# Performance work log

Hardware: AMD Instinct MI355X
Metric: run time of the kernel (lower is better)

## Reference

```python
import jax, jax.numpy as jnp
import numpy as np

B, S, D, H = 2, 2048, 1024, 16
HD = D // H  # head_size = 64

def setup_inputs() -> dict:
    key = jax.random.key(0)
    ks = jax.random.split(key, 8)
    sc = 0.02
    return {
        "q": jax.random.normal(ks[0], (B, S, D), jnp.float32),
        "k": jax.random.normal(ks[1], (B, S, D), jnp.float32),
        "v": jax.random.normal(ks[2], (B, S, D), jnp.float32),
        "padding_mask": jnp.zeros((B, 1, 1, S), jnp.float32),
        "Wq": jax.random.normal(ks[3], (D, D), jnp.float32) * sc,
        "bq": jnp.zeros((D,), jnp.float32),
        "Wk": jax.random.normal(ks[4], (D, D), jnp.float32) * sc,
        "bk": jnp.zeros((D,), jnp.float32),
        "Wv": jax.random.normal(ks[5], (D, D), jnp.float32) * sc,
        "bv": jnp.zeros((D,), jnp.float32),
        "Wo": jax.random.normal(ks[6], (D, D), jnp.float32) * sc,
        "bo": jnp.zeros((D,), jnp.float32),
    }

def reference(q, k, v, padding_mask, Wq, bq, Wk, bk, Wv, bv, Wo, bo):
    b = q.shape[0]
    qh = (q @ Wq + bq).reshape(b, -1, H, HD)
    kh = (k @ Wk + bk).reshape(b, -1, H, HD)
    vh = (v @ Wv + bv).reshape(b, -1, H, HD)
    # [B, H, Sq, Sk] scores, materialized as in the original
    qk = jnp.einsum('bjhd,bkhd->bhjk', qh, kh) / jnp.sqrt(jnp.float32(HD))
    qk = qk + padding_mask * -1e12
    attn = jax.nn.softmax(qk, axis=-1)
    qkv = jnp.einsum('bhjk,bkhd->bjhd', attn, vh).reshape(b, -1, D)
    return qkv @ Wo + bo
```

## Files before the change

kernel.cpp:

```cpp
#include <hip/hip_runtime.h>
#include <math.h>

typedef __bf16 bf16_t;
typedef __bf16 bf16x8 __attribute__((ext_vector_type(8)));
typedef __bf16 bf16x4v __attribute__((ext_vector_type(4)));
typedef float f32x4 __attribute__((ext_vector_type(4)));
typedef float f32x16 __attribute__((ext_vector_type(16)));

#define LOG2E 1.4426950408889634f
#define MBIAS_C (-1e12f * LOG2E)

#if __has_builtin(__builtin_amdgcn_exp2f)
#define EXP2F(x) __builtin_amdgcn_exp2f(x)
#else
#define EXP2F(x) exp2f(x)
#endif

typedef __attribute__((address_space(1))) const unsigned int g_u32;
typedef __attribute__((address_space(3))) unsigned int l_u32;
__device__ __forceinline__ void load_lds_16B(const void* g, void* l){
  __builtin_amdgcn_global_load_lds((g_u32*)g, (l_u32*)l, 16, 0, 0);
}

__device__ __forceinline__ f32x16 zero16(){
  f32x16 z;
  #pragma unroll
  for (int i = 0; i < 16; i++) z[i] = 0.f;
  return z;
}

typedef union { bf16x4v b4; uint2 u2; } pk8;
typedef union { uint2 h[2]; bf16x8 b8; } pk16;
typedef union { float4 f4[4]; f32x16 v; } cinit_t;

__global__ __launch_bounds__(256) void cast3_kernel(const float* __restrict__ q,
                                                    const float* __restrict__ k,
                                                    const float* __restrict__ v,
                                                    bf16_t* __restrict__ out){
  int z = blockIdx.y;
  const float* x = (z == 0) ? q : (z == 1) ? k : v;
  int i = blockIdx.x * 256 + threadIdx.x;
  float4 f = reinterpret_cast<const float4*>(x)[i];
  bf16x4v w;
  w[0] = (bf16_t)f.x; w[1] = (bf16_t)f.y; w[2] = (bf16_t)f.z; w[3] = (bf16_t)f.w;
  reinterpret_cast<bf16x4v*>(out + (size_t)z * 4194304)[i] = w;
}

__global__ __launch_bounds__(256) void mask_scale_kernel(const float* __restrict__ mask,
                                                         float* __restrict__ ms){
  int i = blockIdx.x * 256 + threadIdx.x;
  ms[i] = mask[i] * MBIAS_C;
}

__global__ __launch_bounds__(256) void wtrans4_kernel(const float* __restrict__ Wq,
                                                      const float* __restrict__ Wk,
                                                      const float* __restrict__ Wv,
                                                      const float* __restrict__ Wo,
                                                      bf16_t* __restrict__ Wcat,
                                                      bf16_t* __restrict__ Wot){
  __shared__ float T[32][33];
  int z = blockIdx.z;
  const float* W = (z == 0) ? Wq : (z == 1) ? Wk : (z == 2) ? Wv : Wo;
  bf16_t* dst = (z < 3) ? (Wcat + (size_t)z * 1024 * 1024) : Wot;
  int x = threadIdx.x, y = threadIdx.y;
  int k0 = blockIdx.y * 32, n0 = blockIdx.x * 32;
  #pragma unroll
  for (int i = 0; i < 4; i++) T[y + 8*i][x] = W[(size_t)(k0 + y + 8*i) * 1024 + n0 + x];
  __syncthreads();
  #pragma unroll
  for (int i = 0; i < 4; i++) dst[(size_t)(n0 + y + 8*i) * 1024 + k0 + x] = (bf16_t)T[x][y + 8*i];
}

__device__ __forceinline__ void qkv_epilogue(f32x4 (&acc)[4][4], int seg, int n0g, int m0,
                                             int wm, int wn, int l16, int lq,
                                             const float* bias, bf16_t* qp, bf16_t* kp,
                                             bf16_t* vh){
  bf16_t* Cp = (seg == 0) ? qp : (seg == 1) ? kp : vh;
  float scale = (seg == 0) ? 0.125f * LOG2E : 1.0f;
  #pragma unroll
  for (int ti = 0; ti < 4; ti++){
    #pragma unroll
    for (int tj = 0; tj < 4; tj++){
      int col = (n0g + wn + tj*16 + l16) & 1023;
      float bvv = bias[col];
      #pragma unroll
      for (int r = 0; r < 4; r++){
        int row = m0 + wm + ti*16 + lq*4 + r;
        Cp[(size_t)row * 1024 + col] = (bf16_t)((acc[ti][tj][r] + bvv) * scale);
      }
    }
  }
}

__global__ __launch_bounds__(256) void gemm_qkv_bf(const bf16_t* __restrict__ qkvin,
                                                   const bf16_t* __restrict__ Wcat,
                                                   const float* __restrict__ bq,
                                                   const float* __restrict__ bk,
                                                   const float* __restrict__ bv,
                                                   bf16_t* __restrict__ qp,
                                                   bf16_t* __restrict__ kp,
                                                   bf16_t* __restrict__ vh){
  const int K = 1024;
  __shared__ __align__(16) bf16_t As[128*32];
  __shared__ __align__(16) bf16_t Bs[128*32];
  int tid = threadIdx.x, wave = tid >> 6, lane = tid & 63;
  int l16 = lane & 15, lq = lane >> 4;
  int n0g = blockIdx.x * 128;
  int seg = n0g >> 10;
  const bf16_t* A   = qkvin + (size_t)seg * 4194304;
  const float* bias = (seg == 0) ? bq : (seg == 1) ? bk : bv;
  int m0 = blockIdx.y * 128;
  int wm = (wave >> 1) * 64, wn = (wave & 1) * 64;
  int cposR = lq ^ ((l16 >> 2) & 3);
  f32x4 acc[4][4] = {};
  for (int kt = 0; kt < K; kt += 32){
    __syncthreads();
    #pragma unroll
    for (int i = 0; i < 2; i++){
      int u = tid + 256*i;
      int r = u >> 2, cpos = u & 3, cg = cpos ^ ((r >> 2) & 3);
      int ldsoff = (wave*64 + 256*i) * 16;
      load_lds_16B(&A[(size_t)(m0 + r) * K + kt + cg*8], (char*)As + ldsoff);
      load_lds_16B(&Wcat[(size_t)(n0g + r) * K + kt + cg*8], (char*)Bs + ldsoff);
    }
    __syncthreads();
    bf16x8 af[4], bfr[4];
    #pragma unroll
    for (int t = 0; t < 4; t++) af[t]  = *reinterpret_cast<bf16x8*>(&As[(wm + t*16 + l16)*32 + cposR*8]);
    #pragma unroll
    for (int t = 0; t < 4; t++) bfr[t] = *reinterpret_cast<bf16x8*>(&Bs[(wn + t*16 + l16)*32 + cposR*8]);
    #pragma unroll
    for (int ti = 0; ti < 4; ti++)
      #pragma unroll
      for (int tj = 0; tj < 4; tj++)
        acc[ti][tj] = __builtin_amdgcn_mfma_f32_16x16x32_bf16(af[ti], bfr[tj], acc[ti][tj], 0, 0, 0);
  }
  qkv_epilogue(acc, seg, n0g, m0, wm, wn, l16, lq, bias, qp, kp, vh);
}

__global__ __launch_bounds__(256) void gemm_qkv_f32(const float* __restrict__ qi,
                                                    const float* __restrict__ ki,
                                                    const float* __restrict__ vi,
                                                    const bf16_t* __restrict__ Wcat,
                                                    const float* __restrict__ bq,
                                                    const float* __restrict__ bk,
                                                    const float* __restrict__ bv,
                                                    bf16_t* __restrict__ qp,
                                                    bf16_t* __restrict__ kp,
                                                    bf16_t* __restrict__ vh){
  const int K = 1024;
  __shared__ __align__(16) float  Asf[128*32];
  __shared__ __align__(16) bf16_t Bs[128*32];
  int tid = threadIdx.x, wave = tid >> 6, lane = tid & 63;
  int l16 = lane & 15, lq = lane >> 4;
  int n0g = blockIdx.x * 128;
  int seg = n0g >> 10;
  const float* A    = (seg == 0) ? qi : (seg == 1) ? ki : vi;
  const float* bias = (seg == 0) ? bq : (seg == 1) ? bk : bv;
  int m0 = blockIdx.y * 128;
  int wm = (wave >> 1) * 64, wn = (wave & 1) * 64;
  int cposR = lq ^ ((l16 >> 2) & 3);
  int ca0 = (2*lq)     ^ (l16 & 7);
  int ca1 = (2*lq + 1) ^ (l16 & 7);
  f32x4 acc[4][4] = {};
  for (int kt = 0; kt < K; kt += 32){
    __syncthreads();
    #pragma unroll
    for (int i = 0; i < 4; i++){
      int u = tid + 256*i;
      int r = u >> 3, cpos = u & 7, cg = cpos ^ (r & 7);
      load_lds_16B(&A[(size_t)(m0 + r) * K + kt + cg*4], (char*)Asf + (wave*64 + 256*i)*16);
    }
    #pragma unroll
    for (int i = 0; i < 2; i++){
      int u = tid + 256*i;
      int r = u >> 2, cpos = u & 3, cg = cpos ^ ((r >> 2) & 3);
      load_lds_16B(&Wcat[(size_t)(n0g + r) * K + kt + cg*8], (char*)Bs + (wave*64 + 256*i)*16);
    }
    __syncthreads();
    bf16x8 af[4], bfr[4];
    #pragma unroll
    for (int t = 0; t < 4; t++){
      int row = wm + t*16 + l16;
      f32x4 x0 = *reinterpret_cast<f32x4*>(&Asf[row*32 + ca0*4]);
      f32x4 x1 = *reinterpret_cast<f32x4*>(&Asf[row*32 + ca1*4]);
      bf16x8 a;
      a[0] = (bf16_t)x0[0]; a[1] = (bf16_t)x0[1]; a[2] = (bf16_t)x0[2]; a[3] = (bf16_t)x0[3];
      a[4] = (bf16_t)x1[0]; a[5] = (bf16_t)x1[1]; a[6] = (bf16_t)x1[2]; a[7] = (bf16_t)x1[3];
      af[t] = a;
    }
    #pragma unroll
    for (int t = 0; t < 4; t++) bfr[t] = *reinterpret_cast<bf16x8*>(&Bs[(wn + t*16 + l16)*32 + cposR*8]);
    #pragma unroll
    for (int ti = 0; ti < 4; ti++)
      #pragma unroll
      for (int tj = 0; tj < 4; tj++)
        acc[ti][tj] = __builtin_amdgcn_mfma_f32_16x16x32_bf16(af[ti], bfr[tj], acc[ti][tj], 0, 0, 0);
  }
  qkv_epilogue(acc, seg, n0g, m0, wm, wn, l16, lq, bias, qp, kp, vh);
}

__global__ __launch_bounds__(256) void gemm_out(const bf16_t* __restrict__ A,
                                                const bf16_t* __restrict__ Bt,
                                                const float* __restrict__ bias,
                                                float* __restrict__ C){
  const int K = 1024, N = 1024;
  __shared__ __align__(16) bf16_t As[128*64];
  __shared__ __align__(16) bf16_t Bs[64*64];
  int tid = threadIdx.x, wave = tid >> 6, lane = tid & 63;
  int l16 = lane & 15, lq = lane >> 4;
  int m0 = blockIdx.y * 128, n0 = blockIdx.x * 64;
  int wm = wave * 32;
  f32x4 acc[2][4] = {};
  for (int kt = 0; kt < K; kt += 64){
    __syncthreads();
    #pragma unroll
    for (int i = 0; i < 4; i++){
      int u = tid + 256*i;
      int r = u >> 3, cpos = u & 7, cg = cpos ^ (r & 7);
      load_lds_16B(&A[(size_t)(m0 + r) * K + kt + cg*8], (char*)As + (wave*64 + 256*i)*16);
    }
    #pragma unroll
    for (int i = 0; i < 2; i++){
      int u = tid + 256*i;
      int r = u >> 3, cpos = u & 7, cg = cpos ^ (r & 7);
      load_lds_16B(&Bt[(size_t)(n0 + r) * K + kt + cg*8], (char*)Bs + (wave*64 + 256*i)*16);
    }
    __syncthreads();
    #pragma unroll
    for (int kk = 0; kk < 2; kk++){
      bf16x8 af[2], bfr[4];
      #pragma unroll
      for (int t = 0; t < 2; t++){
        int row = wm + t*16 + l16, cpos = (kk*4 + lq) ^ (l16 & 7);
        af[t] = *reinterpret_cast<bf16x8*>(&As[row*64 + cpos*8]);
      }
      #pragma unroll
      for (int t = 0; t < 4; t++){
        int row = t*16 + l16, cpos = (kk*4 + lq) ^ (l16 & 7);
        bfr[t] = *reinterpret_cast<bf16x8*>(&Bs[row*64 + cpos*8]);
      }
      #pragma unroll
      for (int ti = 0; ti < 2; ti++)
        #pragma unroll
        for (int tj = 0; tj < 4; tj++)
          acc[ti][tj] = __builtin_amdgcn_mfma_f32_16x16x32_bf16(af[ti], bfr[tj], acc[ti][tj], 0, 0, 0);
    }
  }
  #pragma unroll
  for (int ti = 0; ti < 2; ti++){
    #pragma unroll
    for (int tj = 0; tj < 4; tj++){
      int col = n0 + tj*16 + l16;
      float bvv = bias[col];
      #pragma unroll
      for (int r = 0; r < 4; r++){
        int row = m0 + wm + ti*16 + lq*4 + r;
        C[(size_t)row * N + col] = acc[ti][tj][r] + bvv;
      }
    }
  }
}

__global__ __launch_bounds__(256) void vtrans_kernel(const bf16_t* __restrict__ vh,
                                                     bf16_t* __restrict__ Vt){
  __shared__ bf16_t T[64][72];
  int tid = threadIdx.x;
  int s0 = blockIdx.x * 64, h = blockIdx.y, b = blockIdx.z;
  #pragma unroll
  for (int i = 0; i < 2; i++){
    int u = tid + 256*i;
    int r = u >> 3, c = (u & 7) * 8;
    *reinterpret_cast<uint4*>(&T[r][c]) =
      *reinterpret_cast<const uint4*>(&vh[(size_t)(b*2048 + s0 + r) * 1024 + h*64 + c]);
  }
  __syncthreads();
  #pragma unroll
  for (int i = 0; i < 2; i++){
    int u = tid + 256*i;
    int d = u >> 3, cs = (u & 7) * 8;
    bf16_t t8[8];
    #pragma unroll
    for (int j = 0; j < 8; j++) t8[j] = T[cs + j][d];
    *reinterpret_cast<uint4*>(&Vt[(size_t)((b*16 + h)*64 + d) * 2048 + s0 + cs]) =
      *reinterpret_cast<uint4*>(t8);
  }
}

__global__ __launch_bounds__(256, 4) void attn_kernel(const bf16_t* __restrict__ qp,
                                                      const bf16_t* __restrict__ kp,
                                                      const bf16_t* __restrict__ vt,
                                                      const float* __restrict__ ms,
                                                      bf16_t* __restrict__ ctx){
  const int S = 2048, D = 1024, HD = 64;
  __shared__ __align__(16) char smem[33024];
  float* Lsum  = (float*)(smem + 32768);
  float* Opart = (float*)smem;
  int tid = threadIdx.x, wave = tid >> 6, lane = tid & 63;
  int l32 = lane & 31, H = lane >> 5;
  int qhalf = wave & 1, khalf = wave >> 1;
  int qt = blockIdx.x, h = blockIdx.y, b = blockIdx.z;
  const bf16_t* Qg = qp + (size_t)b*S*D + h*HD;
  const bf16_t* Kg = kp + (size_t)b*S*D + h*HD;
  const bf16_t* Vg = vt + (size_t)(b*16 + h)*HD*S;
  const float*  Mg = ms + (size_t)b*S;

  auto stage = [&](int kt, int bsel){
    char* Kd = smem + bsel*8192;
    char* Vd = smem + 16384 + bsel*8192;
    #pragma unroll
    for (int i = 0; i < 2; i++){
      int u = tid + 256*i;
      int r = u >> 3, c = u & 7, cg = c ^ (r & 7);
      int ldsoff = (wave*64 + 256*i) * 16;
      load_lds_16B(&Kg[(size_t)(kt + r) * D + cg*8], Kd + ldsoff);
      load_lds_16B(&Vg[(size_t)r * S + kt + cg*8], Vd + ldsoff);
    }
  };

  int qrow = qt*64 + qhalf*32 + l32;
  bf16x8 qf[4];
  #pragma unroll
  for (int s = 0; s < 4; s++)
    qf[s] = *reinterpret_cast<const bf16x8*>(&Qg[(size_t)qrow * D + s*16 + 8*H]);

  f32x16 o0 = zero16(), o1 = zero16(), lmm = zero16();
  int krow = khalf*32 + l32;

  pk16 ones;
  ones.h[0].x = 0x3F803F80u; ones.h[0].y = 0x3F803F80u;
  ones.h[1].x = 0x3F803F80u; ones.h[1].y = 0x3F803F80u;

  stage(0, 0);
  __syncthreads();
  int cur = 0;

  for (int kt = 0; kt < S; kt += 64){
    cinit_t ci;
    #pragma unroll
    for (int g = 0; g < 4; g++)
      ci.f4[g] = *reinterpret_cast<const float4*>(&Mg[kt + khalf*32 + 8*g + 4*H]);

    if (kt + 64 < S) stage(kt + 64, cur ^ 1);

    bf16_t* Ks  = (bf16_t*)(smem + cur*8192);
    bf16_t* Vts = (bf16_t*)(smem + 16384 + cur*8192);

    f32x16 sc;
    #pragma unroll
    for (int s = 0; s < 4; s++){
      int cp = (2*s + H) ^ (l32 & 7);
      bf16x8 kf = *reinterpret_cast<bf16x8*>(&Ks[krow*64 + cp*8]);
      if (s == 0) sc = __builtin_amdgcn_mfma_f32_32x32x16_bf16(kf, qf[0], ci.v, 0, 0, 0);
      else        sc = __builtin_amdgcn_mfma_f32_32x32x16_bf16(kf, qf[s], sc, 0, 0, 0);
    }
    pk8 grp[4];
    #pragma unroll
    for (int g = 0; g < 4; g++){
      float p0 = EXP2F(sc[4*g+0]);
      float p1 = EXP2F(sc[4*g+1]);
      float p2 = EXP2F(sc[4*g+2]);
      float p3 = EXP2F(sc[4*g+3]);
      pk8 w;
      w.b4[0] = (bf16_t)p0; w.b4[1] = (bf16_t)p1; w.b4[2] = (bf16_t)p2; w.b4[3] = (bf16_t)p3;
      grp[g] = w;
    }
    #pragma unroll
    for (int kk = 0; kk < 2; kk++){
      uint2 ga = grp[2*kk].u2;
      uint2 gb = grp[2*kk+1].u2;
      uint2 send = H ? ga : gb;
      uint2 recv;
      recv.x = (unsigned)__shfl_xor((int)send.x, 32);
      recv.y = (unsigned)__shfl_xor((int)send.y, 32);
      pk16 fr;
      fr.h[0] = H ? recv : ga;
      fr.h[1] = H ? gb : recv;
      int cp = (4*khalf + 2*kk + H) ^ (l32 & 7);
      bf16x8 vf0 = *reinterpret_cast<bf16x8*>(&Vts[l32*64 + cp*8]);
      bf16x8 vf1 = *reinterpret_cast<bf16x8*>(&Vts[(32 + l32)*64 + cp*8]);
      o0  = __builtin_amdgcn_mfma_f32_32x32x16_bf16(fr.b8, vf0, o0, 0, 0, 0);
      o1  = __builtin_amdgcn_mfma_f32_32x32x16_bf16(fr.b8, vf1, o1, 0, 0, 0);
      lmm = __builtin_amdgcn_mfma_f32_32x32x16_bf16(fr.b8, ones.b8, lmm, 0, 0, 0);
    }
    __syncthreads();
    cur ^= 1;
  }

  if (khalf == 1){
    #pragma unroll
    for (int reg = 0; reg < 16; reg++){
      Opart[qhalf*2048 + reg*64 + lane]        = o0[reg];
      Opart[qhalf*2048 + 1024 + reg*64 + lane] = o1[reg];
    }
    if (l32 == 0){
      #pragma unroll
      for (int reg = 0; reg < 16; reg++)
        Lsum[qhalf*32 + (reg & 3) + 8*(reg >> 2) + 4*H] = lmm[reg];
    }
  }
  __syncthreads();
  if (khalf == 0){
    #pragma unroll
    for (int reg = 0; reg < 16; reg++){
      o0[reg] += Opart[qhalf*2048 + reg*64 + lane];
      o1[reg] += Opart[qhalf*2048 + 1024 + reg*64 + lane];
    }
    #pragma unroll
    for (int g = 0; g < 4; g++){
      #pragma unroll
      for (int r = 0; r < 4; r++){
        float lf = lmm[4*g + r] + Lsum[qhalf*32 + 8*g + 4*H + r];
        float inv = 1.f / lf;
        int grow = qt*64 + qhalf*32 + 8*g + 4*H + r;
        size_t base = (size_t)(b*S + grow) * D + h*HD;
        ctx[base + l32]      = (bf16_t)(o0[4*g + r] * inv);
        ctx[base + 32 + l32] = (bf16_t)(o1[4*g + r] * inv);
      }
    }
  }
}

extern "C" void kernel_launch(void* const* d_in, const int* in_sizes, int n_in,
                              void* d_out, int out_size, void* d_ws, size_t ws_size,
                              hipStream_t stream){
  const float* q    = (const float*)d_in[0];
  const float* k    = (const float*)d_in[1];
  const float* v    = (const float*)d_in[2];
  const float* mask = (const float*)d_in[3];
  const float* Wq   = (const float*)d_in[4];
  const float* bq   = (const float*)d_in[5];
  const float* Wk   = (const float*)d_in[6];
  const float* bk   = (const float*)d_in[7];
  const float* Wv   = (const float*)d_in[8];
  const float* bv   = (const float*)d_in[9];
  const float* Wo   = (const float*)d_in[10];
  const float* bo   = (const float*)d_in[11];

  char* ws = (char*)d_ws;
  bf16_t* qp    = (bf16_t*)(ws);
  bf16_t* kp    = (bf16_t*)(ws + 8388608);
  bf16_t* vh    = (bf16_t*)(ws + 16777216);
  bf16_t* Wcat  = (bf16_t*)(ws + 25165824);
  bf16_t* Wot   = (bf16_t*)(ws + 31457280);
  bf16_t* Vt    = (bf16_t*)(ws + 33554432);
  bf16_t* ctx   = (bf16_t*)(ws + 41943040);
  bf16_t* qkvin = (bf16_t*)(ws + 33554432);
  float*  msbuf = (float*)(ws + 16777216);

  wtrans4_kernel<<<dim3(32,32,4), dim3(32,8), 0, stream>>>(Wq, Wk, Wv, Wo, Wcat, Wot);
  if (ws_size >= 58720256){
    cast3_kernel<<<dim3(4096,3), 256, 0, stream>>>(q, k, v, qkvin);
    gemm_qkv_bf<<<dim3(24,32), 256, 0, stream>>>(qkvin, Wcat, bq, bk, bv, qp, kp, vh);
  } else {
    gemm_qkv_f32<<<dim3(24,32), 256, 0, stream>>>(q, k, v, Wcat, bq, bk, bv, qp, kp, vh);
  }
  vtrans_kernel<<<dim3(32,16,2), 256, 0, stream>>>(vh, Vt);
  mask_scale_kernel<<<dim3(16), 256, 0, stream>>>(mask, msbuf);
  attn_kernel<<<dim3(32,16,2), 256, 0, stream>>>(qp, kp, Vt, msbuf, ctx);
  gemm_out<<<dim3(16,32), 256, 0, stream>>>(ctx, Wot, bo, (float*)d_out);
}
```

Measured before the change: 239.3 us.

## Double-buffer GEMM and attention loops, stage mask in LDS as bf16, drop row-sum MFMA

Both GEMMs and the attention kernel get double-buffered LDS with a prefetch of the next tile, explicit vmcnt waits and raw barriers, so global-to-LDS loads overlap MFMA work. The padding mask is stored as bf16 and loaded once into LDS for the whole key range instead of being read from global memory on every tile. The softmax denominator is now summed in scalar registers and combined with a shuffle, which removes the extra MFMA against a ones vector. The change raises LDS use per block and depends on the hand-written vmcnt counts matching the number of outstanding loads.

```diff
diff --git a/kernel.cpp b/kernel.cpp
--- a/kernel.cpp
+++ b/kernel.cpp
@@ -47,9 +47,9 @@
 }
 
 __global__ __launch_bounds__(256) void mask_scale_kernel(const float* __restrict__ mask,
-                                                         float* __restrict__ ms){
+                                                         bf16_t* __restrict__ ms){
   int i = blockIdx.x * 256 + threadIdx.x;
-  ms[i] = mask[i] * MBIAS_C;
+  ms[i] = (bf16_t)(mask[i] * MBIAS_C);
 }
 
 __global__ __launch_bounds__(256) void wtrans4_kernel(const float* __restrict__ Wq,
@@ -101,8 +101,8 @@
                                                    bf16_t* __restrict__ kp,
                                                    bf16_t* __restrict__ vh){
   const int K = 1024;
-  __shared__ __align__(16) bf16_t As[128*32];
-  __shared__ __align__(16) bf16_t Bs[128*32];
+  __shared__ __align__(16) bf16_t As[2][128*32];
+  __shared__ __align__(16) bf16_t Bs[2][128*32];
   int tid = threadIdx.x, wave = tid >> 6, lane = tid & 63;
   int l16 = lane & 15, lq = lane >> 4;
   int n0g = blockIdx.x * 128;
@@ -113,28 +113,49 @@
   int wm = (wave >> 1) * 64, wn = (wave & 1) * 64;
   int cposR = lq ^ ((l16 >> 2) & 3);
   f32x4 acc[4][4] = {};
-  for (int kt = 0; kt < K; kt += 32){
-    __syncthreads();
+
+  auto stage = [&](int kt, int bsel){
     #pragma unroll
     for (int i = 0; i < 2; i++){
       int u = tid + 256*i;
       int r = u >> 2, cpos = u & 3, cg = cpos ^ ((r >> 2) & 3);
       int ldsoff = (wave*64 + 256*i) * 16;
-      load_lds_16B(&A[(size_t)(m0 + r) * K + kt + cg*8], (char*)As + ldsoff);
-      load_lds_16B(&Wcat[(size_t)(n0g + r) * K + kt + cg*8], (char*)Bs + ldsoff);
-    }
-    __syncthreads();
+      load_lds_16B(&A[(size_t)(m0 + r) * K + kt + cg*8], (char*)As[bsel] + ldsoff);
+      load_lds_16B(&Wcat[(size_t)(n0g + r) * K + kt + cg*8], (char*)Bs[bsel] + ldsoff);
+    }
+  };
+  auto compute = [&](int cur){
     bf16x8 af[4], bfr[4];
     #pragma unroll
-    for (int t = 0; t < 4; t++) af[t]  = *reinterpret_cast<bf16x8*>(&As[(wm + t*16 + l16)*32 + cposR*8]);
-    #pragma unroll
-    for (int t = 0; t < 4; t++) bfr[t] = *reinterpret_cast<bf16x8*>(&Bs[(wn + t*16 + l16)*32 + cposR*8]);
+    for (int t = 0; t < 4; t++) af[t]  = *reinterpret_cast<bf16x8*>(&As[cur][(wm + t*16 + l16)*32 + cposR*8]);
+    #pragma unroll
+    for (int t = 0; t < 4; t++) bfr[t] = *reinterpret_cast<bf16x8*>(&Bs[cur][(wn + t*16 + l16)*32 + cposR*8]);
     #pragma unroll
     for (int ti = 0; ti < 4; ti++)
       #pragma unroll
       for (int tj = 0; tj < 4; tj++)
         acc[ti][tj] = __builtin_amdgcn_mfma_f32_16x16x32_bf16(af[ti], bfr[tj], acc[ti][tj], 0, 0, 0);
-  }
+  };
+
+  stage(0, 0);
+  #pragma unroll 1
+  for (int it = 0; it < 31; ++it){
+    stage((it + 1) * 32, (it + 1) & 1);
+    asm volatile("s_waitcnt vmcnt(4)" ::: "memory");
+    __builtin_amdgcn_sched_barrier(0);
+    __builtin_amdgcn_s_barrier();
+    __builtin_amdgcn_sched_barrier(0);
+    compute(it & 1);
+    __builtin_amdgcn_sched_barrier(0);
+    __builtin_amdgcn_s_barrier();
+    __builtin_amdgcn_sched_barrier(0);
+  }
+  asm volatile("s_waitcnt vmcnt(0)" ::: "memory");
+  __builtin_amdgcn_sched_barrier(0);
+  __builtin_amdgcn_s_barrier();
+  __builtin_amdgcn_sched_barrier(0);
+  compute(1);
+
   qkv_epilogue(acc, seg, n0g, m0, wm, wn, l16, lq, bias, qp, kp, vh);
 }
 
@@ -205,40 +226,41 @@
                                                 const float* __restrict__ bias,
                                                 float* __restrict__ C){
   const int K = 1024, N = 1024;
-  __shared__ __align__(16) bf16_t As[128*64];
-  __shared__ __align__(16) bf16_t Bs[64*64];
+  __shared__ __align__(16) bf16_t As[2][128*64];
+  __shared__ __align__(16) bf16_t Bs[2][64*64];
   int tid = threadIdx.x, wave = tid >> 6, lane = tid & 63;
   int l16 = lane & 15, lq = lane >> 4;
   int m0 = blockIdx.y * 128, n0 = blockIdx.x * 64;
   int wm = wave * 32;
   f32x4 acc[2][4] = {};
-  for (int kt = 0; kt < K; kt += 64){
-    __syncthreads();
+
+  auto stage = [&](int kt, int bsel){
     #pragma unroll
     for (int i = 0; i < 4; i++){
       int u = tid + 256*i;
       int r = u >> 3, cpos = u & 7, cg = cpos ^ (r & 7);
-      load_lds_16B(&A[(size_t)(m0 + r) * K + kt + cg*8], (char*)As + (wave*64 + 256*i)*16);
+      load_lds_16B(&A[(size_t)(m0 + r) * K + kt + cg*8], (char*)As[bsel] + (wave*64 + 256*i)*16);
     }
     #pragma unroll
     for (int i = 0; i < 2; i++){
       int u = tid + 256*i;
       int r = u >> 3, cpos = u & 7, cg = cpos ^ (r & 7);
-      load_lds_16B(&Bt[(size_t)(n0 + r) * K + kt + cg*8], (char*)Bs + (wave*64 + 256*i)*16);
-    }
-    __syncthreads();
+      load_lds_16B(&Bt[(size_t)(n0 + r) * K + kt + cg*8], (char*)Bs[bsel] + (wave*64 + 256*i)*16);
+    }
+  };
+  auto compute = [&](int cur){
     #pragma unroll
     for (int kk = 0; kk < 2; kk++){
       bf16x8 af[2], bfr[4];
       #pragma unroll
       for (int t = 0; t < 2; t++){
         int row = wm + t*16 + l16, cpos = (kk*4 + lq) ^ (l16 & 7);
-        af[t] = *reinterpret_cast<bf16x8*>(&As[row*64 + cpos*8]);
+        af[t] = *reinterpret_cast<bf16x8*>(&As[cur][row*64 + cpos*8]);
       }
       #pragma unroll
       for (int t = 0; t < 4; t++){
         int row = t*16 + l16, cpos = (kk*4 + lq) ^ (l16 & 7);
-        bfr[t] = *reinterpret_cast<bf16x8*>(&Bs[row*64 + cpos*8]);
+        bfr[t] = *reinterpret_cast<bf16x8*>(&Bs[cur][row*64 + cpos*8]);
       }
       #pragma unroll
       for (int ti = 0; ti < 2; ti++)
@@ -246,7 +268,27 @@
         for (int tj = 0; tj < 4; tj++)
           acc[ti][tj] = __builtin_amdgcn_mfma_f32_16x16x32_bf16(af[ti], bfr[tj], acc[ti][tj], 0, 0, 0);
     }
-  }
+  };
+
+  stage(0, 0);
+  #pragma unroll 1
+  for (int it = 0; it < 15; ++it){
+    stage((it + 1) * 64, (it + 1) & 1);
+    asm volatile("s_waitcnt vmcnt(6)" ::: "memory");
+    __builtin_amdgcn_sched_barrier(0);
+    __builtin_amdgcn_s_barrier();
+    __builtin_amdgcn_sched_barrier(0);
+    compute(it & 1);
+    __builtin_amdgcn_sched_barrier(0);
+    __builtin_amdgcn_s_barrier();
+    __builtin_amdgcn_sched_barrier(0);
+  }
+  asm volatile("s_waitcnt vmcnt(0)" ::: "memory");
+  __builtin_amdgcn_sched_barrier(0);
+  __builtin_amdgcn_s_barrier();
+  __builtin_amdgcn_sched_barrier(0);
+  compute(1);
+
   #pragma unroll
   for (int ti = 0; ti < 2; ti++){
     #pragma unroll
@@ -290,20 +332,21 @@
 __global__ __launch_bounds__(256, 4) void attn_kernel(const bf16_t* __restrict__ qp,
                                                       const bf16_t* __restrict__ kp,
                                                       const bf16_t* __restrict__ vt,
-                                                      const float* __restrict__ ms,
+                                                      const bf16_t* __restrict__ ms,
                                                       bf16_t* __restrict__ ctx){
   const int S = 2048, D = 1024, HD = 64;
-  __shared__ __align__(16) char smem[33024];
-  float* Lsum  = (float*)(smem + 32768);
+  __shared__ __align__(16) char smem[37376];
+  float* Lsum  = (float*)(smem + 36864);
+  float* Lcomb = (float*)(smem + 37120);
   float* Opart = (float*)smem;
   int tid = threadIdx.x, wave = tid >> 6, lane = tid & 63;
   int l32 = lane & 31, H = lane >> 5;
   int qhalf = wave & 1, khalf = wave >> 1;
   int qt = blockIdx.x, h = blockIdx.y, b = blockIdx.z;
-  const bf16_t* Qg = qp + (size_t)b*S*D + h*HD;
-  const bf16_t* Kg = kp + (size_t)b*S*D + h*HD;
-  const bf16_t* Vg = vt + (size_t)(b*16 + h)*HD*S;
-  const float*  Mg = ms + (size_t)b*S;
+  const bf16_t* Qg  = qp + (size_t)b*S*D + h*HD;
+  const bf16_t* Kg  = kp + (size_t)b*S*D + h*HD;
+  const bf16_t* Vg  = vt + (size_t)(b*16 + h)*HD*S;
+  const bf16_t* Mg2 = ms + (size_t)b*S;
 
   auto stage = [&](int kt, int bsel){
     char* Kd = smem + bsel*8192;
@@ -324,28 +367,26 @@
   for (int s = 0; s < 4; s++)
     qf[s] = *reinterpret_cast<const bf16x8*>(&Qg[(size_t)qrow * D + s*16 + 8*H]);
 
-  f32x16 o0 = zero16(), o1 = zero16(), lmm = zero16();
+  f32x16 o0 = zero16(), o1 = zero16();
+  float lacc = 0.f;
   int krow = khalf*32 + l32;
-
-  pk16 ones;
-  ones.h[0].x = 0x3F803F80u; ones.h[0].y = 0x3F803F80u;
-  ones.h[1].x = 0x3F803F80u; ones.h[1].y = 0x3F803F80u;
-
+  const uint2* mrow = reinterpret_cast<const uint2*>(smem + 32768 + (size_t)(khalf*32 + 4*H)*2);
+
+  load_lds_16B(&Mg2[(size_t)tid*8], smem + 32768 + wave*1024);
   stage(0, 0);
-  __syncthreads();
-  int cur = 0;
-
-  for (int kt = 0; kt < S; kt += 64){
-    cinit_t ci;
-    #pragma unroll
-    for (int g = 0; g < 4; g++)
-      ci.f4[g] = *reinterpret_cast<const float4*>(&Mg[kt + khalf*32 + 8*g + 4*H]);
-
-    if (kt + 64 < S) stage(kt + 64, cur ^ 1);
-
+
+  auto tile_compute = [&](int kt, int cur){
     bf16_t* Ks  = (bf16_t*)(smem + cur*8192);
     bf16_t* Vts = (bf16_t*)(smem + 16384 + cur*8192);
-
+    cinit_t ci;
+    #pragma unroll
+    for (int g = 0; g < 4; g++){
+      uint2 mu = mrow[(kt >> 2) + 2*g];
+      ci.f4[g].x = __uint_as_float(mu.x << 16);
+      ci.f4[g].y = __uint_as_float(mu.x & 0xFFFF0000u);
+      ci.f4[g].z = __uint_as_float(mu.y << 16);
+      ci.f4[g].w = __uint_as_float(mu.y & 0xFFFF0000u);
+    }
     f32x16 sc;
     #pragma unroll
     for (int s = 0; s < 4; s++){
@@ -361,6 +402,7 @@
       float p1 = EXP2F(sc[4*g+1]);
       float p2 = EXP2F(sc[4*g+2]);
       float p3 = EXP2F(sc[4*g+3]);
+      lacc += (p0 + p1) + (p2 + p3);
       pk8 w;
       w.b4[0] = (bf16_t)p0; w.b4[1] = (bf16_t)p1; w.b4[2] = (bf16_t)p2; w.b4[3] = (bf16_t)p3;
       grp[g] = w;
@@ -379,25 +421,38 @@
       int cp = (4*khalf + 2*kk + H) ^ (l32 & 7);
       bf16x8 vf0 = *reinterpret_cast<bf16x8*>(&Vts[l32*64 + cp*8]);
       bf16x8 vf1 = *reinterpret_cast<bf16x8*>(&Vts[(32 + l32)*64 + cp*8]);
-      o0  = __builtin_amdgcn_mfma_f32_32x32x16_bf16(fr.b8, vf0, o0, 0, 0, 0);
-      o1  = __builtin_amdgcn_mfma_f32_32x32x16_bf16(fr.b8, vf1, o1, 0, 0, 0);
-      lmm = __builtin_amdgcn_mfma_f32_32x32x16_bf16(fr.b8, ones.b8, lmm, 0, 0, 0);
-    }
-    __syncthreads();
-    cur ^= 1;
-  }
-
+      o0 = __builtin_amdgcn_mfma_f32_32x32x16_bf16(fr.b8, vf0, o0, 0, 0, 0);
+      o1 = __builtin_amdgcn_mfma_f32_32x32x16_bf16(fr.b8, vf1, o1, 0, 0, 0);
+    }
+  };
+
+  #pragma unroll 1
+  for (int it = 0; it < 31; ++it){
+    stage((it + 1) * 64, (it + 1) & 1);
+    asm volatile("s_waitcnt vmcnt(4)" ::: "memory");
+    __builtin_amdgcn_sched_barrier(0);
+    __builtin_amdgcn_s_barrier();
+    __builtin_amdgcn_sched_barrier(0);
+    tile_compute(it * 64, it & 1);
+    __builtin_amdgcn_sched_barrier(0);
+    __builtin_amdgcn_s_barrier();
+    __builtin_amdgcn_sched_barrier(0);
+  }
+  asm volatile("s_waitcnt vmcnt(0)" ::: "memory");
+  __builtin_amdgcn_sched_barrier(0);
+  __builtin_amdgcn_s_barrier();
+  __builtin_amdgcn_sched_barrier(0);
+  tile_compute(1984, 1);
+
+  float lfull = lacc + __shfl_xor(lacc, 32);
+  __syncthreads();
   if (khalf == 1){
     #pragma unroll
     for (int reg = 0; reg < 16; reg++){
       Opart[qhalf*2048 + reg*64 + lane]        = o0[reg];
       Opart[qhalf*2048 + 1024 + reg*64 + lane] = o1[reg];
     }
-    if (l32 == 0){
-      #pragma unroll
-      for (int reg = 0; reg < 16; reg++)
-        Lsum[qhalf*32 + (reg & 3) + 8*(reg >> 2) + 4*H] = lmm[reg];
-    }
+    if (H == 0) Lsum[qhalf*32 + l32] = lfull;
   }
   __syncthreads();
   if (khalf == 0){
@@ -406,12 +461,14 @@
       o0[reg] += Opart[qhalf*2048 + reg*64 + lane];
       o1[reg] += Opart[qhalf*2048 + 1024 + reg*64 + lane];
     }
+    lfull += Lsum[qhalf*32 + l32];
+    Lcomb[qhalf*32 + l32] = lfull;
     #pragma unroll
     for (int g = 0; g < 4; g++){
+      f32x4 lv = *reinterpret_cast<f32x4*>(&Lcomb[qhalf*32 + 8*g + 4*H]);
       #pragma unroll
       for (int r = 0; r < 4; r++){
-        float lf = lmm[4*g + r] + Lsum[qhalf*32 + 8*g + 4*H + r];
-        float inv = 1.f / lf;
+        float inv = 1.f / lv[r];
         int grow = qt*64 + qhalf*32 + 8*g + 4*H + r;
         size_t base = (size_t)(b*S + grow) * D + h*HD;
         ctx[base + l32]      = (bf16_t)(o0[4*g + r] * inv);
@@ -446,7 +503,7 @@
   bf16_t* Vt    = (bf16_t*)(ws + 33554432);
   bf16_t* ctx   = (bf16_t*)(ws + 41943040);
   bf16_t* qkvin = (bf16_t*)(ws + 33554432);
-  float*  msbuf = (float*)(ws + 16777216);
+  bf16_t* msbuf = (bf16_t*)(ws + 16777216);
 
   wtrans4_kernel<<<dim3(32,32,4), dim3(32,8), 0, stream>>>(Wq, Wk, Wv, Wo, Wcat, Wot);
   if (ws_size >= 58720256){
```

Result: slower. 244.3 us (+2.1%).
